# Kernel tuning notes

Hardware: AMD Instinct MI355X
Metric: run time of the kernel (lower is better)

The kernel has to match this reference:

```python
import jax, jax.numpy as jnp
import numpy as np

TOP_K = 2
TEMP = 1.0

def setup_inputs() -> dict:
    key = jax.random.key(0)
    ks = jax.random.split(key, 7)
    B, T, D, E = 2, 2048, 768, 8
    F = 4 * D
    s = 0.02
    return {
        "x": jax.random.normal(ks[0], (B, T, D), dtype=jnp.float32),
        "gate_w": jax.random.normal(ks[1], (D, E), dtype=jnp.float32) * s,
        "gate_b": jnp.zeros((E,), dtype=jnp.float32),
        "w1": jax.random.normal(ks[2], (E, D, F), dtype=jnp.float32) * s,
        "b1": jnp.zeros((E, F), dtype=jnp.float32),
        "w2": jax.random.normal(ks[3], (E, F, D), dtype=jnp.float32) * s,
        "b2": jnp.zeros((E, D), dtype=jnp.float32),
    }

def reference(x, gate_w, gate_b, w1, b1, w2, b2):
    B, T, D = x.shape
    E = gate_w.shape[1]
    x_flat = x.reshape(-1, D)                       # [N, D]
    logits = x_flat @ gate_w + gate_b              # [N, E]
    gates = jax.nn.softmax(logits / TEMP, axis=-1)
    topk_gates, topk_idx = jax.lax.top_k(gates, TOP_K)   # [N, K]
    topk_gates = topk_gates / (jnp.sum(topk_gates, axis=-1, keepdims=True) + 1e-9)
    # Dense combine weights: w[n, e] = sum_k topk_gates[n, k] * (topk_idx[n, k] == e)
    combine = jnp.sum(
        topk_gates[:, :, None] * jax.nn.one_hot(topk_idx, E, dtype=x.dtype),
        axis=1,
    )                                               # [N, E]
    out = jnp.zeros_like(x_flat)
    for e in range(E):  # fixed small expert loop (structurally distinct params)
        h = jax.nn.gelu(x_flat @ w1[e] + b1[e], approximate=False)  # [N, 4D]
        y = h @ w2[e] + b2[e]                                       # [N, D]
        out = out + combine[:, e:e + 1] * y
    return out.reshape(B, T, D)
```

## Files before the change

kernel.cpp:

```cpp
#include <hip/hip_runtime.h>
#include <hip/hip_bf16.h>


#define N_TOK 4096
#define DIM   768
#define FDIM  3072
#define NEXP  8

typedef __attribute__((ext_vector_type(8))) _Float16 f16x8;
typedef __attribute__((ext_vector_type(4))) _Float16 f16x4;
typedef __attribute__((ext_vector_type(4))) float     f32x4;

__device__ __forceinline__ float gelu_exact(float v) {
    return 0.5f * v * (1.0f + erff(v * 0.7071067811865475f));
}

__global__ __launch_bounds__(256) void cast_x_kernel(const float* __restrict__ x,
                                                     _Float16* __restrict__ xh) {
    int i = blockIdx.x * 256 + threadIdx.x;
    float4 v = ((const float4*)x)[i];
    f16x4 o;
    o[0] = (_Float16)v.x; o[1] = (_Float16)v.y;
    o[2] = (_Float16)v.z; o[3] = (_Float16)v.w;
    ((f16x4*)xh)[i] = o;
}

__global__ __launch_bounds__(256) void transpose_cast_kernel(const float* __restrict__ in,
                                                             _Float16* __restrict__ out,
                                                             int R, int C) {
    const int e  = blockIdx.z;
    const size_t eoff = (size_t)e * R * C;
    const int c0 = blockIdx.x * 64;
    const int r0 = blockIdx.y * 64;
    __shared__ _Float16 tile[64][66];
    const int t = threadIdx.x;
    #pragma unroll
    for (int it = 0; it < 4; it++) {
        int lin = it * 256 + t;
        int r  = lin >> 4;
        int c4 = lin & 15;
        float4 v = *(const float4*)&in[eoff + (size_t)(r0 + r) * C + c0 + c4 * 4];
        tile[r][c4 * 4 + 0] = (_Float16)v.x;
        tile[r][c4 * 4 + 1] = (_Float16)v.y;
        tile[r][c4 * 4 + 2] = (_Float16)v.z;
        tile[r][c4 * 4 + 3] = (_Float16)v.w;
    }
    __syncthreads();
    #pragma unroll
    for (int it = 0; it < 4; it++) {
        int lin = it * 256 + t;
        int c  = lin >> 4;
        int r4 = lin & 15;
        f16x4 o;
        #pragma unroll
        for (int j = 0; j < 4; j++) o[j] = tile[r4 * 4 + j][c];
        *(f16x4*)&out[eoff + (size_t)(c0 + c) * R + r0 + r4 * 4] = o;
    }
}

__global__ __launch_bounds__(256) void gate_kernel(const float* __restrict__ x,
                                                   const float* __restrict__ gw,
                                                   const float* __restrict__ gb,
                                                   int* __restrict__ tok_list,
                                                   float* __restrict__ wt_list,
                                                   int* __restrict__ count) {
    const int gtid = blockIdx.x * 256 + threadIdx.x;
    const int n    = gtid >> 6;
    const int lane = threadIdx.x & 63;
    if (n >= N_TOK) return;
    double part[NEXP];
    #pragma unroll
    for (int e = 0; e < NEXP; e++) part[e] = 0.0;
    for (int d = lane; d < DIM; d += 64) {
        float xv = x[n * DIM + d];
        const float* g = &gw[d * NEXP];
        #pragma unroll
        for (int e = 0; e < NEXP; e++) part[e] += (double)xv * (double)g[e];
    }
    #pragma unroll
    for (int e = 0; e < NEXP; e++) {
        double v = part[e];
        #pragma unroll
        for (int off = 32; off > 0; off >>= 1) v += __shfl_xor(v, off);
        part[e] = v + (double)gb[e];
    }
    if (lane == 0) {
        double mx = part[0];
        #pragma unroll
        for (int e = 1; e < NEXP; e++) mx = fmax(mx, part[e]);
        double ex[NEXP]; double s = 0.0;
        #pragma unroll
        for (int e = 0; e < NEXP; e++) { ex[e] = exp(part[e] - mx); s += ex[e]; }
        int i0 = 0;
        #pragma unroll
        for (int e = 1; e < NEXP; e++) if (ex[e] > ex[i0]) i0 = e;
        int i1 = (i0 == 0) ? 1 : 0;
        #pragma unroll
        for (int e = 0; e < NEXP; e++) if (e != i0 && ex[e] > ex[i1]) i1 = e;
        float g0 = (float)(ex[i0] / s), g1 = (float)(ex[i1] / s);
        float dn = g0 + g1 + 1e-9f;
        float w0 = g0 / dn, w1 = g1 / dn;
        int s0 = atomicAdd(&count[i0], 1);
        tok_list[i0 * N_TOK + s0] = n;  wt_list[i0 * N_TOK + s0] = w0;
        int s1 = atomicAdd(&count[i1], 1);
        tok_list[i1 * N_TOK + s1] = n;  wt_list[i1 * N_TOK + s1] = w1;
    }
}

__global__ void scan_kernel(const int* __restrict__ count, int* __restrict__ basep) {
    if (threadIdx.x == 0) {
        int s = 0;
        for (int e = 0; e < NEXP; e++) { basep[e] = s; s += count[e]; }
    }
}

__global__ __launch_bounds__(256) void mm1_kernel(const _Float16* __restrict__ xh,
                                                  const _Float16* __restrict__ w1t,
                                                  const float* __restrict__ bias1,
                                                  const int* __restrict__ tok_list,
                                                  const int* __restrict__ count,
                                                  const int* __restrict__ basep,
                                                  _Float16* __restrict__ h) {
    const int e    = blockIdx.z;
    const int cnt  = count[e];
    const int row0 = blockIdx.y * 128;
    if (row0 >= cnt) return;
    const int col0 = blockIdx.x * 128;
    const int t    = threadIdx.x;
    const int lane = t & 63;
    const int wv   = t >> 6;
    const int wy   = wv >> 1, wx = wv & 1;
    const int m_lane = lane & 15, quad = lane >> 4;

    __shared__ __align__(16) _Float16 As[128][32];
    __shared__ __align__(16) _Float16 Bs[128][32];

    const int srow = t >> 2;
    const int kin  = (t & 3) * 8;

    int i0 = row0 + srow;      if (i0 > cnt - 1) i0 = cnt - 1;
    int i1 = row0 + 64 + srow; if (i1 > cnt - 1) i1 = cnt - 1;
    const int tokA0 = tok_list[e * N_TOK + i0];
    const int tokA1 = tok_list[e * N_TOK + i1];
    const _Float16* pa0 = xh + (size_t)tokA0 * DIM + kin;
    const _Float16* pa1 = xh + (size_t)tokA1 * DIM + kin;
    const _Float16* pb0 = w1t + (size_t)e * FDIM * DIM + (size_t)(col0 + srow) * DIM + kin;
    const _Float16* pb1 = pb0 + (size_t)64 * DIM;

    f32x4 acc[4][4];
    #pragma unroll
    for (int i = 0; i < 4; i++)
        #pragma unroll
        for (int j = 0; j < 4; j++)
            acc[i][j] = (f32x4){0.f, 0.f, 0.f, 0.f};

    for (int kk = 0; kk < DIM; kk += 32) {
        uint4 a0 = *(const uint4*)(pa0 + kk);
        uint4 a1 = *(const uint4*)(pa1 + kk);
        uint4 b0 = *(const uint4*)(pb0 + kk);
        uint4 b1 = *(const uint4*)(pb1 + kk);
        __syncthreads();
        *(uint4*)&As[srow][kin]      = a0;
        *(uint4*)&As[64 + srow][kin] = a1;
        *(uint4*)&Bs[srow][kin]      = b0;
        *(uint4*)&Bs[64 + srow][kin] = b1;
        __syncthreads();
        f16x8 af[4], bf[4];
        #pragma unroll
        for (int i = 0; i < 4; i++)
            af[i] = *(const f16x8*)&As[wy * 64 + i * 16 + m_lane][quad * 8];
        #pragma unroll
        for (int j = 0; j < 4; j++)
            bf[j] = *(const f16x8*)&Bs[wx * 64 + j * 16 + m_lane][quad * 8];
        #pragma unroll
        for (int i = 0; i < 4; i++)
            #pragma unroll
            for (int j = 0; j < 4; j++)
                acc[i][j] = __builtin_amdgcn_mfma_f32_16x16x32_f16(af[i], bf[j], acc[i][j], 0, 0, 0);
    }

    const int hbase = basep[e];
    #pragma unroll
    for (int i = 0; i < 4; i++) {
        #pragma unroll
        for (int r = 0; r < 4; r++) {
            int rl = wy * 64 + i * 16 + quad * 4 + r;
            int gr = row0 + rl;
            if (gr < cnt) {
                _Float16* hrow = h + (size_t)(hbase + gr) * FDIM;
                #pragma unroll
                for (int j = 0; j < 4; j++) {
                    int c = col0 + wx * 64 + j * 16 + m_lane;
                    float v = acc[i][j][r] + bias1[e * FDIM + c];
                    hrow[c] = (_Float16)gelu_exact(v);
                }
            }
        }
    }
}

__global__ __launch_bounds__(256) void mm2_kernel(const _Float16* __restrict__ h,
                                                  const _Float16* __restrict__ w2t,
                                                  const float* __restrict__ bias2,
                                                  const int* __restrict__ tok_list,
                                                  const float* __restrict__ wt_list,
                                                  const int* __restrict__ count,
                                                  const int* __restrict__ basep,
                                                  float* __restrict__ out) {
    const int e    = blockIdx.z;
    const int cnt  = count[e];
    const int row0 = blockIdx.y * 128;
    if (row0 >= cnt) return;
    const int col0 = blockIdx.x * 128;
    const int t    = threadIdx.x;
    const int lane = t & 63;
    const int wv   = t >> 6;
    const int wy   = wv >> 1, wx = wv & 1;
    const int m_lane = lane & 15, quad = lane >> 4;

    __shared__ __align__(16) _Float16 As[128][32];
    __shared__ __align__(16) _Float16 Bs[128][32];

    const int srow = t >> 2;
    const int kin  = (t & 3) * 8;

    const int hbase = basep[e];
    int i0 = row0 + srow;      if (i0 > cnt - 1) i0 = cnt - 1;
    int i1 = row0 + 64 + srow; if (i1 > cnt - 1) i1 = cnt - 1;
    const _Float16* pa0 = h + (size_t)(hbase + i0) * FDIM + kin;
    const _Float16* pa1 = h + (size_t)(hbase + i1) * FDIM + kin;
    const _Float16* pb0 = w2t + (size_t)e * DIM * FDIM + (size_t)(col0 + srow) * FDIM + kin;
    const _Float16* pb1 = pb0 + (size_t)64 * FDIM;

    f32x4 acc[4][4];
    #pragma unroll
    for (int i = 0; i < 4; i++)
        #pragma unroll
        for (int j = 0; j < 4; j++)
            acc[i][j] = (f32x4){0.f, 0.f, 0.f, 0.f};

    for (int kk = 0; kk < FDIM; kk += 32) {
        uint4 a0 = *(const uint4*)(pa0 + kk);
        uint4 a1 = *(const uint4*)(pa1 + kk);
        uint4 b0 = *(const uint4*)(pb0 + kk);
        uint4 b1 = *(const uint4*)(pb1 + kk);
        __syncthreads();
        *(uint4*)&As[srow][kin]      = a0;
        *(uint4*)&As[64 + srow][kin] = a1;
        *(uint4*)&Bs[srow][kin]      = b0;
        *(uint4*)&Bs[64 + srow][kin] = b1;
        __syncthreads();
        f16x8 af[4], bf[4];
        #pragma unroll
        for (int i = 0; i < 4; i++)
            af[i] = *(const f16x8*)&As[wy * 64 + i * 16 + m_lane][quad * 8];
        #pragma unroll
        for (int j = 0; j < 4; j++)
            bf[j] = *(const f16x8*)&Bs[wx * 64 + j * 16 + m_lane][quad * 8];
        #pragma unroll
        for (int i = 0; i < 4; i++)
            #pragma unroll
            for (int j = 0; j < 4; j++)
                acc[i][j] = __builtin_amdgcn_mfma_f32_16x16x32_f16(af[i], bf[j], acc[i][j], 0, 0, 0);
    }

    #pragma unroll
    for (int i = 0; i < 4; i++) {
        #pragma unroll
        for (int r = 0; r < 4; r++) {
            int rl = wy * 64 + i * 16 + quad * 4 + r;
            int gr = row0 + rl;
            if (gr < cnt) {
                int tok   = tok_list[e * N_TOK + gr];
                float wgt = wt_list[e * N_TOK + gr];
                float* orow = out + (size_t)tok * DIM;
                #pragma unroll
                for (int j = 0; j < 4; j++) {
                    int c = col0 + wx * 64 + j * 16 + m_lane;
                    float v = acc[i][j][r] + bias2[e * DIM + c];
                    atomicAdd(&orow[c], wgt * v);
                }
            }
        }
    }
}

extern "C" void kernel_launch(void* const* d_in, const int* in_sizes, int n_in,
                              void* d_out, int out_size, void* d_ws, size_t ws_size,
                              hipStream_t stream) {
    const float* x  = (const float*)d_in[0];
    const float* gw = (const float*)d_in[1];
    const float* gb = (const float*)d_in[2];
    const float* w1 = (const float*)d_in[3];
    const float* b1 = (const float*)d_in[4];
    const float* w2 = (const float*)d_in[5];
    const float* b2 = (const float*)d_in[6];
    float* out = (float*)d_out;

    char* ws = (char*)d_ws;
    _Float16* xh   = (_Float16*)ws;
    _Float16* w1t  = xh  + (size_t)N_TOK * DIM;
    _Float16* w2t  = w1t + (size_t)NEXP * FDIM * DIM;
    _Float16* hbuf = w2t + (size_t)NEXP * DIM * FDIM;
    int*   tok_list = (int*)(hbuf + (size_t)2 * N_TOK * FDIM);
    float* wt_list  = (float*)(tok_list + NEXP * N_TOK);
    int*   count    = (int*)(wt_list + NEXP * N_TOK);
    int*   basep    = count + 8;

    hipMemsetAsync(count, 0, 64, stream);
    hipMemsetAsync(out, 0, (size_t)out_size * sizeof(float), stream);

    cast_x_kernel<<<dim3(N_TOK * DIM / 4 / 256), 256, 0, stream>>>(x, xh);
    transpose_cast_kernel<<<dim3(FDIM / 64, DIM / 64, NEXP), 256, 0, stream>>>(w1, w1t, DIM, FDIM);
    transpose_cast_kernel<<<dim3(DIM / 64, FDIM / 64, NEXP), 256, 0, stream>>>(w2, w2t, FDIM, DIM);
    gate_kernel<<<dim3(N_TOK / 4), 256, 0, stream>>>(x, gw, gb, tok_list, wt_list, count);
    scan_kernel<<<1, 64, 0, stream>>>(count, basep);
    mm1_kernel<<<dim3(FDIM / 128, N_TOK / 128, NEXP), 256, 0, stream>>>(
        xh, w1t, b1, tok_list, count, basep, hbuf);
    mm2_kernel<<<dim3(DIM / 128, N_TOK / 128, NEXP), 256, 0, stream>>>(
        hbuf, w2t, b2, tok_list, wt_list, count, basep, out);
}
```

Measured before the change: 532.7 us.

## Load GEMM tiles directly into LDS with fragment-ordered layout

Replaces the register-staged global-to-LDS copies in both expert GEMM kernels with direct global_load_lds transfers. The LDS tiles are relaid out so each 16-row block is stored in MFMA fragment order, and each lane reads 16 contiguous bytes at lane*8. The goal is to remove VGPR staging and LDS bank conflicts on the fragment reads. It keeps the single-buffered loop with a full vmcnt wait, so load latency is still exposed, and it relies on the builtin placing each lane's 16 bytes at consecutive LDS offsets.

```diff
diff --git a/kernel.cpp b/kernel.cpp
--- a/kernel.cpp
+++ b/kernel.cpp
@@ -13,6 +13,12 @@
 
 __device__ __forceinline__ float gelu_exact(float v) {
     return 0.5f * v * (1.0f + erff(v * 0.7071067811865475f));
+}
+
+__device__ __forceinline__ void gl_lds16(const _Float16* g, _Float16* l) {
+    __builtin_amdgcn_global_load_lds(
+        (const __attribute__((address_space(1))) unsigned int*)g,
+        (__attribute__((address_space(3))) unsigned int*)l, 16, 0, 0);
 }
 
 __global__ __launch_bounds__(256) void cast_x_kernel(const float* __restrict__ x,
@@ -132,20 +138,23 @@
     const int wy   = wv >> 1, wx = wv & 1;
     const int m_lane = lane & 15, quad = lane >> 4;
 
-    __shared__ __align__(16) _Float16 As[128][32];
-    __shared__ __align__(16) _Float16 Bs[128][32];
-
-    const int srow = t >> 2;
-    const int kin  = (t & 3) * 8;
-
-    int i0 = row0 + srow;      if (i0 > cnt - 1) i0 = cnt - 1;
-    int i1 = row0 + 64 + srow; if (i1 > cnt - 1) i1 = cnt - 1;
-    const int tokA0 = tok_list[e * N_TOK + i0];
-    const int tokA1 = tok_list[e * N_TOK + i1];
-    const _Float16* pa0 = xh + (size_t)tokA0 * DIM + kin;
-    const _Float16* pa1 = xh + (size_t)tokA1 * DIM + kin;
-    const _Float16* pb0 = w1t + (size_t)e * FDIM * DIM + (size_t)(col0 + srow) * DIM + kin;
-    const _Float16* pb1 = pb0 + (size_t)64 * DIM;
+    __shared__ __align__(16) _Float16 As[4096];
+    __shared__ __align__(16) _Float16 Bs[4096];
+
+    const int b0 = wv * 2, b1 = b0 + 1;
+    int ra0 = row0 + b0 * 16 + m_lane; if (ra0 > cnt - 1) ra0 = cnt - 1;
+    int ra1 = row0 + b1 * 16 + m_lane; if (ra1 > cnt - 1) ra1 = cnt - 1;
+    const int tokA0 = tok_list[e * N_TOK + ra0];
+    const int tokA1 = tok_list[e * N_TOK + ra1];
+    const _Float16* pa0 = xh + (size_t)tokA0 * DIM + quad * 8;
+    const _Float16* pa1 = xh + (size_t)tokA1 * DIM + quad * 8;
+    const _Float16* pb0 = w1t + (size_t)e * FDIM * DIM
+                        + (size_t)(col0 + b0 * 16 + m_lane) * DIM + quad * 8;
+    const _Float16* pb1 = pb0 + (size_t)16 * DIM;
+    _Float16* la0 = &As[b0 * 512];
+    _Float16* la1 = &As[b1 * 512];
+    _Float16* lb0 = &Bs[b0 * 512];
+    _Float16* lb1 = &Bs[b1 * 512];
 
     f32x4 acc[4][4];
     #pragma unroll
@@ -155,23 +164,20 @@
             acc[i][j] = (f32x4){0.f, 0.f, 0.f, 0.f};
 
     for (int kk = 0; kk < DIM; kk += 32) {
-        uint4 a0 = *(const uint4*)(pa0 + kk);
-        uint4 a1 = *(const uint4*)(pa1 + kk);
-        uint4 b0 = *(const uint4*)(pb0 + kk);
-        uint4 b1 = *(const uint4*)(pb1 + kk);
         __syncthreads();
-        *(uint4*)&As[srow][kin]      = a0;
-        *(uint4*)&As[64 + srow][kin] = a1;
-        *(uint4*)&Bs[srow][kin]      = b0;
-        *(uint4*)&Bs[64 + srow][kin] = b1;
+        gl_lds16(pa0 + kk, la0);
+        gl_lds16(pa1 + kk, la1);
+        gl_lds16(pb0 + kk, lb0);
+        gl_lds16(pb1 + kk, lb1);
+        asm volatile("s_waitcnt vmcnt(0)" ::: "memory");
         __syncthreads();
         f16x8 af[4], bf[4];
         #pragma unroll
         for (int i = 0; i < 4; i++)
-            af[i] = *(const f16x8*)&As[wy * 64 + i * 16 + m_lane][quad * 8];
+            af[i] = *(const f16x8*)&As[(wy * 4 + i) * 512 + lane * 8];
         #pragma unroll
         for (int j = 0; j < 4; j++)
-            bf[j] = *(const f16x8*)&Bs[wx * 64 + j * 16 + m_lane][quad * 8];
+            bf[j] = *(const f16x8*)&Bs[(wx * 4 + j) * 512 + lane * 8];
         #pragma unroll
         for (int i = 0; i < 4; i++)
             #pragma unroll
@@ -218,19 +224,22 @@
     const int wy   = wv >> 1, wx = wv & 1;
     const int m_lane = lane & 15, quad = lane >> 4;
 
-    __shared__ __align__(16) _Float16 As[128][32];
-    __shared__ __align__(16) _Float16 Bs[128][32];
-
-    const int srow = t >> 2;
-    const int kin  = (t & 3) * 8;
+    __shared__ __align__(16) _Float16 As[4096];
+    __shared__ __align__(16) _Float16 Bs[4096];
 
     const int hbase = basep[e];
-    int i0 = row0 + srow;      if (i0 > cnt - 1) i0 = cnt - 1;
-    int i1 = row0 + 64 + srow; if (i1 > cnt - 1) i1 = cnt - 1;
-    const _Float16* pa0 = h + (size_t)(hbase + i0) * FDIM + kin;
-    const _Float16* pa1 = h + (size_t)(hbase + i1) * FDIM + kin;
-    const _Float16* pb0 = w2t + (size_t)e * DIM * FDIM + (size_t)(col0 + srow) * FDIM + kin;
-    const _Float16* pb1 = pb0 + (size_t)64 * FDIM;
+    const int b0 = wv * 2, b1 = b0 + 1;
+    int ra0 = row0 + b0 * 16 + m_lane; if (ra0 > cnt - 1) ra0 = cnt - 1;
+    int ra1 = row0 + b1 * 16 + m_lane; if (ra1 > cnt - 1) ra1 = cnt - 1;
+    const _Float16* pa0 = h + (size_t)(hbase + ra0) * FDIM + quad * 8;
+    const _Float16* pa1 = h + (size_t)(hbase + ra1) * FDIM + quad * 8;
+    const _Float16* pb0 = w2t + (size_t)e * DIM * FDIM
+                        + (size_t)(col0 + b0 * 16 + m_lane) * FDIM + quad * 8;
+    const _Float16* pb1 = pb0 + (size_t)16 * FDIM;
+    _Float16* la0 = &As[b0 * 512];
+    _Float16* la1 = &As[b1 * 512];
+    _Float16* lb0 = &Bs[b0 * 512];
+    _Float16* lb1 = &Bs[b1 * 512];
 
     f32x4 acc[4][4];
     #pragma unroll
@@ -240,23 +249,20 @@
             acc[i][j] = (f32x4){0.f, 0.f, 0.f, 0.f};
 
     for (int kk = 0; kk < FDIM; kk += 32) {
-        uint4 a0 = *(const uint4*)(pa0 + kk);
-        uint4 a1 = *(const uint4*)(pa1 + kk);
-        uint4 b0 = *(const uint4*)(pb0 + kk);
-        uint4 b1 = *(const uint4*)(pb1 + kk);
         __syncthreads();
-        *(uint4*)&As[srow][kin]      = a0;
-        *(uint4*)&As[64 + srow][kin] = a1;
-        *(uint4*)&Bs[srow][kin]      = b0;
-        *(uint4*)&Bs[64 + srow][kin] = b1;
+        gl_lds16(pa0 + kk, la0);
+        gl_lds16(pa1 + kk, la1);
+        gl_lds16(pb0 + kk, lb0);
+        gl_lds16(pb1 + kk, lb1);
+        asm volatile("s_waitcnt vmcnt(0)" ::: "memory");
         __syncthreads();
         f16x8 af[4], bf[4];
         #pragma unroll
         for (int i = 0; i < 4; i++)
-            af[i] = *(const f16x8*)&As[wy * 64 + i * 16 + m_lane][quad * 8];
+            af[i] = *(const f16x8*)&As[(wy * 4 + i) * 512 + lane * 8];
         #pragma unroll
         for (int j = 0; j < 4; j++)
-            bf[j] = *(const f16x8*)&Bs[wx * 64 + j * 16 + m_lane][quad * 8];
+            bf[j] = *(const f16x8*)&Bs[(wx * 4 + j) * 512 + lane * 8];
         #pragma unroll
         for (int i = 0; i < 4; i++)
             #pragma unroll
```

Result: slower. 591.6 us (+11.1%).
